# Kernel tuning notes

Measured on AMD Instinct MI355X. Metric: run time of the kernel, lower is better.

Reference implementation:

```python
import jax, jax.numpy as jnp
import numpy as np

B, T, D, H, E, R, M, HID, NB = 8, 832, 1024, 16, 16, 8, 16, 4096, 576
LORA_SCALE = 1.0 / R  # alpha / rank


def _ln(x, g, b, eps=1e-6):
    m = x.mean(-1, keepdims=True)
    v = ((x - m) ** 2).mean(-1, keepdims=True)
    return (x - m) / jnp.sqrt(v + eps) * g + b


def setup_inputs() -> dict:
    key = jax.random.key(0)
    ks = jax.random.split(key, 12)
    sd = 0.02
    return {
        's': jax.random.normal(ks[0], (B, T, D), jnp.float32),
        'attn_mask': jnp.zeros((1, 1, T, T), jnp.float32),
        'g1': jnp.ones((D,), jnp.float32),
        'b1': jnp.zeros((D,), jnp.float32),
        'w_qkv': jax.random.normal(ks[1], (D, 3 * D), jnp.float32) * sd,
        'b_qkv': jnp.zeros((3 * D,), jnp.float32),
        'w_proj': jax.random.normal(ks[2], (D, D), jnp.float32) * sd,
        'b_proj': jnp.zeros((D,), jnp.float32),
        'g2': jnp.ones((D,), jnp.float32),
        'b2': jnp.zeros((D,), jnp.float32),
        'w_fc1': jax.random.normal(ks[3], (D, HID), jnp.float32) * sd,
        'b_fc1': jnp.zeros((HID,), jnp.float32),
        'w_fc2': jax.random.normal(ks[4], (HID, D), jnp.float32) * sd,
        'b_fc2': jnp.zeros((D,), jnp.float32),
        'lora_A': jax.random.normal(ks[5], (E, D, R), jnp.float32) * sd,
        'lora_B': jax.random.normal(ks[6], (E, R, D), jnp.float32) * sd,
        'active_expert_indices': jnp.arange(E, dtype=jnp.int32),
        'num_backbone_tokens': NB,
    }


def reference(s, attn_mask, g1, b1, w_qkv, b_qkv, w_proj, b_proj,
              g2, b2, w_fc1, b_fc1, w_fc2, b_fc2, lora_A, lora_B,
              active_expert_indices, num_backbone_tokens):
    Bb, Tt, Dd = s.shape
    hd = Dd // H
    # --- shared attention ---
    x = _ln(s, g1, b1)
    qkv = (x @ w_qkv + b_qkv).reshape(Bb, Tt, 3, H, hd).transpose(2, 0, 3, 1, 4)
    q, k, v = qkv[0], qkv[1], qkv[2]  # [B,H,T,hd]
    scores = jnp.einsum('bhqd,bhkd->bhqk', q * (hd ** -0.5), k) + attn_mask
    p = jax.nn.softmax(scores, axis=-1)
    o = jnp.einsum('bhqk,bhkd->bhqd', p, v).transpose(0, 2, 1, 3).reshape(Bb, Tt, Dd)
    s = s + (o @ w_proj + b_proj)
    # --- shared MLP ---
    s_norm = _ln(s, g2, b2)
    shared = jax.nn.gelu(s_norm @ w_fc1 + b_fc1, approximate=False) @ w_fc2 + b_fc2
    # --- per-expert LoRA on expert token segment ---
    nb = num_backbone_tokens
    z = s_norm[:, nb:, :].reshape(Bb, -1, M, Dd)  # [B,K,M,D]
    Ak = lora_A[active_expert_indices]            # [K,D,R]
    Bk = lora_B[active_expert_indices]            # [K,R,D]
    down = jnp.einsum('bkmd,kdr->bkmr', z, Ak)
    up = jnp.einsum('bkmr,krd->bkmd', down, Bk) * LORA_SCALE
    shared = shared.at[:, nb:, :].add(up.reshape(Bb, -1, Dd))
    return s + shared
```

## Files before the change

### kernel.cpp

```cpp
#include <hip/hip_runtime.h>
#include <hip/hip_bf16.h>
#include <math.h>

typedef unsigned short u16;
typedef __attribute__((ext_vector_type(8))) short short8;
typedef __attribute__((ext_vector_type(4))) float f32x4;

constexpr int B_ = 8, T_ = 832, D_ = 1024, H_ = 16, HID_ = 4096, NB_ = 576;
constexpr int NT_ = B_ * T_;

__device__ inline u16 f2b(float f) {
    union { float f; unsigned u; } x{f};
    unsigned r = (x.u + 0x7FFFu + ((x.u >> 16) & 1u)) >> 16;
    return (u16)r;
}
__device__ inline float b2f(u16 b) {
    union { unsigned u; float f; } x; x.u = ((unsigned)b) << 16; return x.f;
}

__device__ inline float erf_inl(float x) {
    float ax = fabsf(x);
    float t = __frcp_rn(1.0f + 0.3275911f * ax);
    float p = 1.061405429f;
    p = p * t - 1.453152027f;
    p = p * t + 1.421413741f;
    p = p * t - 0.284496736f;
    p = p * t + 0.254829592f;
    p = p * t;
    float e = 1.0f - p * __expf(-ax * ax);
    return copysignf(e, x);
}

__device__ inline void gload_lds16(const void* g, void* l) {
    __builtin_amdgcn_global_load_lds((const __attribute__((address_space(1))) void*)g,
                                     (__attribute__((address_space(3))) void*)l, 16, 0, 0);
}

__global__ __launch_bounds__(256) void wtrans_kernel(const float* __restrict__ in,
                                                     u16* __restrict__ out, int K, int N) {
    __shared__ u16 tile[32][34];
    int n0 = blockIdx.x * 32, k0 = blockIdx.y * 32;
    int tx = threadIdx.x & 31, ty = threadIdx.x >> 5;
    for (int i = 0; i < 4; i++) {
        int k = k0 + ty + i * 8;
        tile[ty + i * 8][tx] = f2b(in[(size_t)k * N + n0 + tx]);
    }
    __syncthreads();
    for (int i = 0; i < 4; i++) {
        int n = n0 + ty + i * 8;
        out[(size_t)n * K + k0 + tx] = tile[tx][ty + i * 8];
    }
}

__global__ __launch_bounds__(256) void ln_kernel(const float* __restrict__ x,
                                                 const float* __restrict__ g,
                                                 const float* __restrict__ bt,
                                                 u16* __restrict__ out) {
    int row = blockIdx.x, tid = threadIdx.x;
    float4 v = ((const float4*)(x + (size_t)row * D_))[tid];
    float s = v.x + v.y + v.z + v.w;
    float q = v.x * v.x + v.y * v.y + v.z * v.z + v.w * v.w;
    for (int o = 1; o < 64; o <<= 1) { s += __shfl_xor(s, o); q += __shfl_xor(q, o); }
    __shared__ float red[4][2];
    if ((tid & 63) == 0) { red[tid >> 6][0] = s; red[tid >> 6][1] = q; }
    __syncthreads();
    s = red[0][0] + red[1][0] + red[2][0] + red[3][0];
    q = red[0][1] + red[1][1] + red[2][1] + red[3][1];
    float mean = s * (1.0f / D_);
    float var = q * (1.0f / D_) - mean * mean;
    float inv = rsqrtf(fmaxf(var, 0.f) + 1e-6f);
    float4 gv = ((const float4*)g)[tid];
    float4 bv = ((const float4*)bt)[tid];
    u16* orow = out + (size_t)row * D_ + tid * 4;
    orow[0] = f2b((v.x - mean) * inv * gv.x + bv.x);
    orow[1] = f2b((v.y - mean) * inv * gv.y + bv.y);
    orow[2] = f2b((v.z - mean) * inv * gv.z + bv.z);
    orow[3] = f2b((v.w - mean) * inv * gv.w + bv.w);
}

template<int BM, int BN, int WR, int WC, int MODE>
__global__ __launch_bounds__(WR * WC * 64, (WR * WC == 8) ? 2 : 3)
void gemm3(const u16* __restrict__ A, const u16* __restrict__ Bt,
           const float* __restrict__ bias, const float* __restrict__ resid,
           void* __restrict__ outp, int M, int N, int K) {
    constexpr int THREADS = WR * WC * 64;
    constexpr int MF = BM / WR / 16;
    constexpr int NF = BN / WC / 16;
    constexpr int NROWS = BM + BN;
    constexpr int CHUNKS = NROWS * 4 / THREADS;
    constexpr int LDSU = NROWS * 32;
    __shared__ u16 lds_[3 * LDSU];

    int tid = threadIdx.x, l = tid & 63, w = tid >> 6;
    int lrow = l & 15, lgrp = l >> 4;
    int wr = w / WC, wc = w % WC;

    int nwg = gridDim.x * gridDim.y;
    int bid = blockIdx.y * gridDim.x + blockIdx.x;
    int cpx = nwg >> 3;
    int swz = (bid & 7) * cpx + (bid >> 3);
    int bx = swz % gridDim.x, by = swz / gridDim.x;
    int m0 = by * BM, n0 = bx * BN;

    const u16* src[CHUNKS];
    int ldst[CHUNKS];
    for (int i = 0; i < CHUNKS; i++) {
        int c = i * THREADS + tid;
        int lc = (c & ~7) | ((c ^ (c >> 3)) & 7);
        int row = lc >> 2, colu = (lc & 3) * 8;
        src[i] = (row < BM) ? A + (size_t)(m0 + row) * K + colu
                            : Bt + (size_t)(n0 + row - BM) * K + colu;
        ldst[i] = c * 8;
    }

#define STAGE3(bufi, kt)                                                    \
    do {                                                                    \
        int kof = (kt) * 32;                                                \
        u16* bb = lds_ + (bufi) * LDSU;                                     \
        for (int i = 0; i < CHUNKS; i++) gload_lds16(src[i] + kof, bb + ldst[i]); \
    } while (0)

    f32x4 acc[MF][NF];
    for (int m = 0; m < MF; m++) for (int n = 0; n < NF; n++) acc[m][n] = (f32x4){0, 0, 0, 0};

    int aidx[MF], bidx[NF];
    for (int m = 0; m < MF; m++) {
        int row = wr * 64 + m * 16 + lrow;
        aidx[m] = (row * 32 + lgrp * 8) ^ (((row >> 1) & 7) << 3);
    }
    for (int n = 0; n < NF; n++) {
        int row = BM + wc * 64 + n * 16 + lrow;
        bidx[n] = (row * 32 + lgrp * 8) ^ (((row >> 1) & 7) << 3);
    }

    int nkt = K >> 5;
    STAGE3(0, 0);
    STAGE3(1, 1);
    if constexpr (CHUNKS == 3) asm volatile("s_waitcnt vmcnt(3)" ::: "memory");
    else                       asm volatile("s_waitcnt vmcnt(4)" ::: "memory");
    asm volatile("s_barrier" ::: "memory");

    int cur = 0;
    for (int t = 0; t < nkt; ++t) {
        int sb = cur + 2; if (sb >= 3) sb -= 3;
        if (t + 2 < nkt) STAGE3(sb, t + 2);

        const u16* bp = lds_ + cur * LDSU;
        short8 af[MF], bfr[NF];
        for (int m = 0; m < MF; m++) af[m] = *(const short8*)(bp + aidx[m]);
        for (int n = 0; n < NF; n++) bfr[n] = *(const short8*)(bp + bidx[n]);

        __builtin_amdgcn_s_setprio(1);
        for (int m = 0; m < MF; m++)
            for (int n = 0; n < NF; n++)
                acc[m][n] = __builtin_amdgcn_mfma_f32_16x16x32_bf16(af[m], bfr[n], acc[m][n], 0, 0, 0);
        __builtin_amdgcn_s_setprio(0);

        if (t + 2 < nkt) {
            if constexpr (CHUNKS == 3) asm volatile("s_waitcnt vmcnt(3)" ::: "memory");
            else                       asm volatile("s_waitcnt vmcnt(4)" ::: "memory");
        } else if (t + 1 < nkt) {
            asm volatile("s_waitcnt vmcnt(0)" ::: "memory");
        }
        asm volatile("s_barrier" ::: "memory");
        cur = cur + 1; if (cur == 3) cur = 0;
    }
#undef STAGE3

    for (int m = 0; m < MF; m++) {
        int rbase = m0 + wr * 64 + m * 16 + lgrp * 4;
        for (int n = 0; n < NF; n++) {
            int col = n0 + wc * 64 + n * 16 + lrow;
            float bv = bias[col];
            for (int j = 0; j < 4; j++) {
                int row = rbase + j;
                float v = acc[m][n][j] + bv;
                size_t off = (size_t)row * N + col;
                if constexpr (MODE == 0) {
                    ((u16*)outp)[off] = f2b(v);
                } else if constexpr (MODE == 1) {
                    ((float*)outp)[off] = v + resid[off];
                } else {
                    float gl = 0.5f * v * (1.0f + erf_inl(v * 0.70710678118654752f));
                    ((u16*)outp)[off] = f2b(gl);
                }
            }
        }
    }
}

__global__ __launch_bounds__(256) void vtrans_kernel(const u16* __restrict__ qkv,
                                                     u16* __restrict__ vt) {
    __shared__ u16 tile[32][66];
    int bh = blockIdx.y, b = bh >> 4, h = bh & 15;
    int t0 = blockIdx.x * 32;
    int dx = threadIdx.x & 63, ty = threadIdx.x >> 6;
    for (int i = 0; i < 8; i++) {
        int tt = ty * 8 + i;
        tile[tt][dx] = qkv[(size_t)(b * T_ + t0 + tt) * 3072 + 2048 + h * 64 + dx];
    }
    __syncthreads();
    int tx = threadIdx.x & 31, dy = threadIdx.x >> 5;
    for (int i = 0; i < 8; i++) {
        int d = dy * 8 + i;
        vt[((size_t)bh * 64 + d) * T_ + t0 + tx] = tile[tx][d];
    }
}

__global__ __launch_bounds__(512, 4) void attn_kernel(const u16* __restrict__ qkv,
                                                      const u16* __restrict__ vt,
                                                      const float* __restrict__ mask,
                                                      u16* __restrict__ obuf) {
    __shared__ u16 Ks[2][4096];
    __shared__ u16 Vs[2][4096];
    __shared__ u16 Ps[8][1024];
    int qt = blockIdx.x, bh = blockIdx.y, b = bh >> 4, h = bh & 15;
    int tid = threadIdx.x, w = tid >> 6, l = tid & 63;
    int lrow = l & 15, lgrp = l >> 4;

    int qrow = qt * 128 + w * 16 + lrow;
    int qrc = qrow < T_ ? qrow : T_ - 1;
    const u16* qp = qkv + (size_t)(b * T_ + qrc) * 3072 + h * 64 + lgrp * 8;
    short8 aq0, aq1;
    {
        short8 r0 = *(const short8*)qp;
        short8 r1 = *(const short8*)(qp + 32);
        for (int i = 0; i < 8; i++) {
            aq0[i] = (short)f2b(b2f((u16)r0[i]) * 0.125f);
            aq1[i] = (short)f2b(b2f((u16)r1[i]) * 0.125f);
        }
    }

    int tq0 = qt * 128 + w * 16 + lgrp * 4;
    bool qvalid = tq0 < T_;
    const float* mrowp[4];
#pragma unroll
    for (int j = 0; j < 4; j++) {
        int tq = tq0 + j; if (tq >= T_) tq = T_ - 1;
        mrowp[j] = mask + (size_t)tq * T_;
    }

    float m_r[4], l_r[4];
    f32x4 oacc[4];
    for (int j = 0; j < 4; j++) { m_r[j] = -1e30f; l_r[j] = 0.f; }
    for (int n = 0; n < 4; n++) oacc[n] = (f32x4){0, 0, 0, 0};

    int srow = tid >> 3, sp = tid & 7;
    int se = (sp ^ (srow & 7)) * 8;
    const u16* kbase = qkv + (size_t)b * T_ * 3072 + 1024 + h * 64;
    const u16* vbase = vt + (size_t)bh * 64 * T_;

#define STAGE_KV(buf, kk0)                                                        \
    do {                                                                          \
        gload_lds16(kbase + (size_t)((kk0) + srow) * 3072 + se, &Ks[buf][w * 512]); \
        gload_lds16(vbase + (size_t)srow * T_ + (kk0) + se, &Vs[buf][w * 512]);     \
    } while (0)

    float mc[16], mn[16];
    STAGE_KV(0, 0);
#pragma unroll
    for (int j = 0; j < 4; j++)
#pragma unroll
        for (int c = 0; c < 4; c++)
            mc[j * 4 + c] = mrowp[j][c * 16 + lrow];
    __syncthreads();

    int cur = 0;
    u16* Pw = Ps[w];
    int swl = lrow & 7;
    int slot0 = (lgrp ^ swl) * 8, slot1 = ((lgrp + 4) ^ swl) * 8;

    for (int kt = 0; kt < 13; ++kt) {
        int kk0 = kt * 64;
        if (kt < 12) {
            STAGE_KV(cur ^ 1, kk0 + 64);
#pragma unroll
            for (int j = 0; j < 4; j++)
#pragma unroll
                for (int c = 0; c < 4; c++)
                    mn[j * 4 + c] = mrowp[j][kk0 + 64 + c * 16 + lrow];
        }

        f32x4 sc[4];
        for (int c = 0; c < 4; c++) sc[c] = (f32x4){0, 0, 0, 0};
        const u16* Kb = Ks[cur];
        __builtin_amdgcn_s_setprio(1);
        for (int c = 0; c < 4; c++) {
            const u16* krow = Kb + (c * 16 + lrow) * 64;
            short8 bk0 = *(const short8*)(krow + slot0);
            short8 bk1 = *(const short8*)(krow + slot1);
            sc[c] = __builtin_amdgcn_mfma_f32_16x16x32_bf16(aq0, bk0, sc[c], 0, 0, 0);
            sc[c] = __builtin_amdgcn_mfma_f32_16x16x32_bf16(aq1, bk1, sc[c], 0, 0, 0);
        }
        __builtin_amdgcn_s_setprio(0);

        int lo3 = lrow & 7, hi = lrow >> 3;
#pragma unroll
        for (int j = 0; j < 4; j++) {
            float s0 = sc[0][j] + mc[j * 4 + 0];
            float s1 = sc[1][j] + mc[j * 4 + 1];
            float s2 = sc[2][j] + mc[j * 4 + 2];
            float s3 = sc[3][j] + mc[j * 4 + 3];
            float mx = fmaxf(fmaxf(s0, s1), fmaxf(s2, s3));
            mx = fmaxf(mx, __shfl_xor(mx, 1));
            mx = fmaxf(mx, __shfl_xor(mx, 2));
            mx = fmaxf(mx, __shfl_xor(mx, 4));
            mx = fmaxf(mx, __shfl_xor(mx, 8));
            float mnew = fmaxf(m_r[j], mx);
            float scf = __expf(m_r[j] - mnew);
            float p0 = __expf(s0 - mnew), p1 = __expf(s1 - mnew);
            float p2 = __expf(s2 - mnew), p3 = __expf(s3 - mnew);
            float ps = (p0 + p1) + (p2 + p3);
            ps += __shfl_xor(ps, 1); ps += __shfl_xor(ps, 2);
            ps += __shfl_xor(ps, 4); ps += __shfl_xor(ps, 8);
            l_r[j] = l_r[j] * scf + ps;
            m_r[j] = mnew;
            for (int n = 0; n < 4; n++) oacc[n][j] *= scf;
            int row_p = lgrp * 4 + j, swp = row_p & 7;
            u16* pr = Pw + row_p * 64;
            pr[((hi ^ swp) * 8) + lo3]       = f2b(p0);
            pr[(((2 + hi) ^ swp) * 8) + lo3] = f2b(p1);
            pr[(((4 + hi) ^ swp) * 8) + lo3] = f2b(p2);
            pr[(((6 + hi) ^ swp) * 8) + lo3] = f2b(p3);
        }

        short8 ap0 = *(const short8*)&Pw[lrow * 64 + slot0];
        short8 ap1 = *(const short8*)&Pw[lrow * 64 + slot1];
        const u16* Vb = Vs[cur];
        __builtin_amdgcn_s_setprio(1);
        for (int n = 0; n < 4; n++) {
            const u16* vrow = Vb + (n * 16 + lrow) * 64;
            short8 bv0 = *(const short8*)(vrow + slot0);
            short8 bv1 = *(const short8*)(vrow + slot1);
            oacc[n] = __builtin_amdgcn_mfma_f32_16x16x32_bf16(ap0, bv0, oacc[n], 0, 0, 0);
            oacc[n] = __builtin_amdgcn_mfma_f32_16x16x32_bf16(ap1, bv1, oacc[n], 0, 0, 0);
        }
        __builtin_amdgcn_s_setprio(0);

        __syncthreads();
#pragma unroll
        for (int i = 0; i < 16; i++) mc[i] = mn[i];
        cur ^= 1;
    }
#undef STAGE_KV

    if (qvalid) {
        for (int j = 0; j < 4; j++) {
            float inv = 1.0f / l_r[j];
            int t = tq0 + j;
            for (int n = 0; n < 4; n++)
                obuf[(size_t)(b * T_ + t) * 1024 + h * 64 + n * 16 + lrow] = f2b(oacc[n][j] * inv);
        }
    }
}

__global__ __launch_bounds__(256) void lora_kernel(const u16* __restrict__ snorm,
                                                   const float* __restrict__ lA,
                                                   const float* __restrict__ lB,
                                                   const int* __restrict__ idx,
                                                   float* __restrict__ outp) {
    __shared__ float down[16][8];
    int blk = blockIdx.x, b = blk >> 4, kk = blk & 15;
    int e = idx[kk];
    int tok0 = b * T_ + NB_ + kk * 16;
    int tid = threadIdx.x;
    if (tid < 128) {
        int m = tid >> 3, r = tid & 7;
        const u16* z = snorm + (size_t)(tok0 + m) * D_;
        const float* Ae = lA + (size_t)e * D_ * 8 + r;
        float acc = 0.f;
        for (int d = 0; d < D_; ++d) acc += b2f(z[d]) * Ae[(size_t)d * 8];
        down[m][r] = acc;
    }
    __syncthreads();
    for (int ci = 0; ci < 4; ci++) {
        int col = tid + ci * 256;
        float br[8];
        for (int r = 0; r < 8; r++) br[r] = lB[((size_t)e * 8 + r) * D_ + col];
        for (int m = 0; m < 16; m++) {
            float acc = 0.f;
            for (int r = 0; r < 8; r++) acc += down[m][r] * br[r];
            outp[(size_t)(tok0 + m) * D_ + col] += acc * 0.125f;
        }
    }
}

extern "C" void kernel_launch(void* const* d_in, const int* in_sizes, int n_in,
                              void* d_out, int out_size, void* d_ws, size_t ws_size,
                              hipStream_t stream) {
    const float* s      = (const float*)d_in[0];
    const float* mask   = (const float*)d_in[1];
    const float* g1     = (const float*)d_in[2];
    const float* b1     = (const float*)d_in[3];
    const float* w_qkv  = (const float*)d_in[4];
    const float* b_qkv  = (const float*)d_in[5];
    const float* w_proj = (const float*)d_in[6];
    const float* b_proj = (const float*)d_in[7];
    const float* g2     = (const float*)d_in[8];
    const float* b2     = (const float*)d_in[9];
    const float* w_fc1  = (const float*)d_in[10];
    const float* b_fc1  = (const float*)d_in[11];
    const float* w_fc2  = (const float*)d_in[12];
    const float* b_fc2  = (const float*)d_in[13];
    const float* lA     = (const float*)d_in[14];
    const float* lB     = (const float*)d_in[15];
    const int*   eidx   = (const int*)d_in[16];
    float* out = (float*)d_out;
    char* ws = (char*)d_ws;

    u16*   wqkvT = (u16*)(ws + 0);
    u16*   wprojT= (u16*)(ws + 6291456);
    u16*   wfc1T = (u16*)(ws + 8388608);
    u16*   wfc2T = (u16*)(ws + 16777216);
    float* s1    = (float*)(ws + 25165824);
    u16*   xln   = (u16*)(ws + 52428800);
    u16*   vt    = (u16*)(ws + 66060288);
    u16*   qkv   = (u16*)(ws + 79691776);
    u16*   h     = (u16*)(ws + 66060288);

    wtrans_kernel<<<dim3(3072 / 32, 1024 / 32), 256, 0, stream>>>(w_qkv, wqkvT, 1024, 3072);
    wtrans_kernel<<<dim3(1024 / 32, 1024 / 32), 256, 0, stream>>>(w_proj, wprojT, 1024, 1024);
    wtrans_kernel<<<dim3(4096 / 32, 1024 / 32), 256, 0, stream>>>(w_fc1, wfc1T, 1024, 4096);
    wtrans_kernel<<<dim3(1024 / 32, 4096 / 32), 256, 0, stream>>>(w_fc2, wfc2T, 4096, 1024);

    ln_kernel<<<NT_, 256, 0, stream>>>(s, g1, b1, xln);
    gemm3<128, 256, 2, 4, 0><<<dim3(3072 / 256, NT_ / 128), 512, 0, stream>>>(xln, wqkvT, b_qkv, nullptr, qkv, NT_, 3072, 1024);
    vtrans_kernel<<<dim3(26, 128), 256, 0, stream>>>(qkv, vt);
    attn_kernel<<<dim3(7, 128), 512, 0, stream>>>(qkv, vt, mask, xln);
    gemm3<128, 128, 2, 2, 1><<<dim3(1024 / 128, NT_ / 128), 256, 0, stream>>>(xln, wprojT, b_proj, s, s1, NT_, 1024, 1024);
    ln_kernel<<<NT_, 256, 0, stream>>>(s1, g2, b2, xln);
    gemm3<128, 256, 2, 4, 2><<<dim3(4096 / 256, NT_ / 128), 512, 0, stream>>>(xln, wfc1T, b_fc1, nullptr, h, NT_, 4096, 1024);
    gemm3<128, 128, 2, 2, 1><<<dim3(1024 / 128, NT_ / 128), 256, 0, stream>>>(h, wfc2T, b_fc2, s1, out, NT_, 1024, 4096);
    lora_kernel<<<128, 256, 0, stream>>>(xln, lA, lB, eidx, out);
}
```

Before: 431.3 us.

## Merge weight transposes into one launch, unroll GEMM loops, split LoRA down-projection

Replaces four weight-transpose launches with a single kernel that picks the matrix from the flat block index, cutting launch overhead and tail gaps. Adds explicit unroll pragmas throughout the GEMM staging, fragment-load, MFMA and epilogue loops so arrays stay in registers. Splits the LoRA down-projection reduction across all 256 threads with a shuffle combine instead of 128 threads doing full-length serial loops. Unrolling may raise register pressure in the GEMM.

New measurement: 412.0 us. 1.05x faster.

```diff
diff --git a/kernel.cpp b/kernel.cpp
--- a/kernel.cpp
+++ b/kernel.cpp
@@ -36,10 +36,21 @@
                                      (__attribute__((address_space(3))) void*)l, 16, 0, 0);
 }
 
-__global__ __launch_bounds__(256) void wtrans_kernel(const float* __restrict__ in,
-                                                     u16* __restrict__ out, int K, int N) {
+__global__ __launch_bounds__(256) void wtrans_all(const float* __restrict__ wq,
+                                                  const float* __restrict__ wp,
+                                                  const float* __restrict__ w1,
+                                                  const float* __restrict__ w2,
+                                                  u16* __restrict__ oq, u16* __restrict__ op,
+                                                  u16* __restrict__ o1, u16* __restrict__ o2) {
     __shared__ u16 tile[32][34];
-    int n0 = blockIdx.x * 32, k0 = blockIdx.y * 32;
+    int bid = blockIdx.x;
+    const float* in; u16* out; int K, N, idx;
+    if (bid < 3072)      { in = wq; out = oq; K = 1024; N = 3072; idx = bid; }
+    else if (bid < 4096) { in = wp; out = op; K = 1024; N = 1024; idx = bid - 3072; }
+    else if (bid < 8192) { in = w1; out = o1; K = 1024; N = 4096; idx = bid - 4096; }
+    else                 { in = w2; out = o2; K = 4096; N = 1024; idx = bid - 8192; }
+    int nx = N >> 5;
+    int n0 = (idx % nx) * 32, k0 = (idx / nx) * 32;
     int tx = threadIdx.x & 31, ty = threadIdx.x >> 5;
     for (int i = 0; i < 4; i++) {
         int k = k0 + ty + i * 8;
@@ -104,6 +115,7 @@
 
     const u16* src[CHUNKS];
     int ldst[CHUNKS];
+#pragma unroll
     for (int i = 0; i < CHUNKS; i++) {
         int c = i * THREADS + tid;
         int lc = (c & ~7) | ((c ^ (c >> 3)) & 7);
@@ -117,17 +129,23 @@
     do {                                                                    \
         int kof = (kt) * 32;                                                \
         u16* bb = lds_ + (bufi) * LDSU;                                     \
+        _Pragma("unroll")                                                   \
         for (int i = 0; i < CHUNKS; i++) gload_lds16(src[i] + kof, bb + ldst[i]); \
     } while (0)
 
     f32x4 acc[MF][NF];
-    for (int m = 0; m < MF; m++) for (int n = 0; n < NF; n++) acc[m][n] = (f32x4){0, 0, 0, 0};
+#pragma unroll
+    for (int m = 0; m < MF; m++)
+#pragma unroll
+        for (int n = 0; n < NF; n++) acc[m][n] = (f32x4){0, 0, 0, 0};
 
     int aidx[MF], bidx[NF];
+#pragma unroll
     for (int m = 0; m < MF; m++) {
         int row = wr * 64 + m * 16 + lrow;
         aidx[m] = (row * 32 + lgrp * 8) ^ (((row >> 1) & 7) << 3);
     }
+#pragma unroll
     for (int n = 0; n < NF; n++) {
         int row = BM + wc * 64 + n * 16 + lrow;
         bidx[n] = (row * 32 + lgrp * 8) ^ (((row >> 1) & 7) << 3);
@@ -147,11 +165,15 @@
 
         const u16* bp = lds_ + cur * LDSU;
         short8 af[MF], bfr[NF];
+#pragma unroll
         for (int m = 0; m < MF; m++) af[m] = *(const short8*)(bp + aidx[m]);
+#pragma unroll
         for (int n = 0; n < NF; n++) bfr[n] = *(const short8*)(bp + bidx[n]);
 
         __builtin_amdgcn_s_setprio(1);
+#pragma unroll
         for (int m = 0; m < MF; m++)
+#pragma unroll
             for (int n = 0; n < NF; n++)
                 acc[m][n] = __builtin_amdgcn_mfma_f32_16x16x32_bf16(af[m], bfr[n], acc[m][n], 0, 0, 0);
         __builtin_amdgcn_s_setprio(0);
@@ -167,11 +189,14 @@
     }
 #undef STAGE3
 
+#pragma unroll
     for (int m = 0; m < MF; m++) {
         int rbase = m0 + wr * 64 + m * 16 + lgrp * 4;
+#pragma unroll
         for (int n = 0; n < NF; n++) {
             int col = n0 + wc * 64 + n * 16 + lrow;
             float bv = bias[col];
+#pragma unroll
             for (int j = 0; j < 4; j++) {
                 int row = rbase + j;
                 float v = acc[m][n][j] + bv;
@@ -364,13 +389,16 @@
     int e = idx[kk];
     int tok0 = b * T_ + NB_ + kk * 16;
     int tid = threadIdx.x;
-    if (tid < 128) {
-        int m = tid >> 3, r = tid & 7;
-        const u16* z = snorm + (size_t)(tok0 + m) * D_;
-        const float* Ae = lA + (size_t)e * D_ * 8 + r;
+    {
+        int m = tid >> 4;
+        int r = (tid >> 1) & 7;
+        int dh = tid & 1;
+        const u16* z = snorm + (size_t)(tok0 + m) * D_ + dh * 512;
+        const float* Ae = lA + (size_t)e * D_ * 8 + (size_t)(dh * 512) * 8 + r;
         float acc = 0.f;
-        for (int d = 0; d < D_; ++d) acc += b2f(z[d]) * Ae[(size_t)d * 8];
-        down[m][r] = acc;
+        for (int d = 0; d < 512; ++d) acc += b2f(z[d]) * Ae[(size_t)d * 8];
+        acc += __shfl_xor(acc, 1);
+        if (dh == 0) down[m][r] = acc;
     }
     __syncthreads();
     for (int ci = 0; ci < 4; ci++) {
@@ -418,11 +446,8 @@
     u16*   qkv   = (u16*)(ws + 79691776);
     u16*   h     = (u16*)(ws + 66060288);
 
-    wtrans_kernel<<<dim3(3072 / 32, 1024 / 32), 256, 0, stream>>>(w_qkv, wqkvT, 1024, 3072);
-    wtrans_kernel<<<dim3(1024 / 32, 1024 / 32), 256, 0, stream>>>(w_proj, wprojT, 1024, 1024);
-    wtrans_kernel<<<dim3(4096 / 32, 1024 / 32), 256, 0, stream>>>(w_fc1, wfc1T, 1024, 4096);
-    wtrans_kernel<<<dim3(1024 / 32, 4096 / 32), 256, 0, stream>>>(w_fc2, wfc2T, 4096, 1024);
-
+    wtrans_all<<<12288, 256, 0, stream>>>(w_qkv, w_proj, w_fc1, w_fc2,
+                                          wqkvT, wprojT, wfc1T, wfc2T);
     ln_kernel<<<NT_, 256, 0, stream>>>(s, g1, b1, xln);
     gemm3<128, 256, 2, 4, 0><<<dim3(3072 / 256, NT_ / 128), 512, 0, stream>>>(xln, wqkvT, b_qkv, nullptr, qkv, NT_, 3072, 1024);
     vtrans_kernel<<<dim3(26, 128), 256, 0, stream>>>(qkv, vt);
```
